# Optimization experiments

Measured on AMD Instinct MI355X. Metric: run time of the kernel, lower is better.

The kernel has to match this reference:

```python
import jax, jax.numpy as jnp
import numpy as np

E = 8       # num_experts
TOP_K = 2
H = 512     # hidden_size
DFF = 2048  # expert FFN inner dim (4*H)
B, S = 4, 2048


def setup_inputs() -> dict:
    key = jax.random.key(0)
    k0, k1, k2, k3 = jax.random.split(key, 4)
    return {
        "hidden_states": jax.random.normal(k0, (B, S, H), jnp.float32),
        # router gate: kaiming-ish init scaled by 0.01 (near-uniform routing)
        "gate_w": jax.random.normal(k1, (E, H), jnp.float32) * 0.01,
        "w1": jax.random.normal(k2, (E, H, DFF), jnp.float32) * (1.0 / np.sqrt(H)),
        "b1": jnp.zeros((E, DFF), jnp.float32),
        "w2": jax.random.normal(k3, (E, DFF, H), jnp.float32) * (1.0 / np.sqrt(DFF)),
        "b2": jnp.zeros((E, H), jnp.float32),
    }


def reference(hidden_states, gate_w, w1, b1, w2, b2):
    # hidden_states: (B, S, H)
    b, s, h = hidden_states.shape
    flat = hidden_states.reshape(-1, h)                 # (T, H), T = B*S

    # --- TopKRouter (eval mode: no gaussian noise) ---
    logits = flat @ gate_w.T                            # (T, E)
    top_vals, top_idx = jax.lax.top_k(logits, TOP_K)    # (T, K)
    top_w = jax.nn.softmax(top_vals, axis=-1)           # softmax over selected k only

    # combine[t, e] = routing weight of expert e for token t (0 if not selected).
    # top_k indices are distinct per token, so summing over k matches the
    # original masked scatter-add output[mask] += weight * expert_out.
    combine = jnp.sum(
        jax.nn.one_hot(top_idx, E, dtype=flat.dtype) * top_w[..., None], axis=1
    )                                                   # (T, E)

    # --- experts: dense compute per expert, weighted combine ---
    out = jnp.zeros_like(flat)
    for e in range(E):  # fixed small loop over experts (not a data dim)
        hdn = jax.nn.gelu(flat @ w1[e] + b1[e])         # (T, DFF)
        out = out + combine[:, e:e + 1] * (hdn @ w2[e] + b2[e])
    return out.reshape(b, s, h)
```

## Files before the change

kernel.cpp:

```cpp
#include <hip/hip_runtime.h>
#include <hip/hip_bf16.h>

#define E_    8
#define H_    512
#define DFF_  2048
#define T_    8192
#define NSLOT (2 * T_)

typedef float  f32x4  __attribute__((ext_vector_type(4)));
typedef short  bf16x8 __attribute__((ext_vector_type(8)));

static __device__ __forceinline__ ushort f2bf(float f) {
  union { float f; unsigned u; } v; v.f = f;
  unsigned r = v.u + 0x7FFFu + ((v.u >> 16) & 1u);
  return (ushort)(r >> 16);
}

static __device__ __forceinline__ void gload16(const void* g, void* l) {
  __builtin_amdgcn_global_load_lds((const __attribute__((address_space(1))) void*)g,
                                   (__attribute__((address_space(3))) void*)l, 16, 0, 0);
}

static __device__ __forceinline__ void transpose_body(
    const float* __restrict__ in, ushort* __restrict__ out, int R, int C,
    int bx, int by, int e, float tile[64][65], int t) {
  int r0 = by * 64, c0 = bx * 64;
  int row = t >> 2, seg = t & 3;
  const float* src = in + ((size_t)e * R + r0 + row) * C + c0 + seg * 16;
#pragma unroll
  for (int i = 0; i < 4; ++i) {
    float4 v = *(const float4*)(src + i * 4);
    tile[row][seg * 16 + i * 4 + 0] = v.x;
    tile[row][seg * 16 + i * 4 + 1] = v.y;
    tile[row][seg * 16 + i * 4 + 2] = v.z;
    tile[row][seg * 16 + i * 4 + 3] = v.w;
  }
  __syncthreads();
  int c = t >> 2;
  ushort vals[16];
#pragma unroll
  for (int j = 0; j < 16; ++j) vals[j] = f2bf(tile[seg * 16 + j][c]);
  ushort* dst = out + ((size_t)e * C + c0 + c) * R + r0 + seg * 16;
  *(uint4*)(dst)     = *(uint4*)&vals[0];
  *(uint4*)(dst + 8) = *(uint4*)&vals[8];
}

__global__ void prep_kernel(const float* __restrict__ x, const float* __restrict__ gw,
                            const float* __restrict__ w1, const float* __restrict__ w2,
                            ushort* __restrict__ xb, float* __restrict__ slotw,
                            int* __restrict__ slote, ushort* __restrict__ w1t,
                            ushort* __restrict__ w2t, float* __restrict__ out) {
  __shared__ float tile[64][65];
  int bid = blockIdx.x;
  int tid = threadIdx.x;
  if (bid < 2048) {
    int tokn = bid * 4 + (tid >> 6);
    int lane = tid & 63;
    const float4* xr = (const float4*)(x + (size_t)tokn * H_ + lane * 8);
    float4 x0 = xr[0], x1 = xr[1];
    ushort v[8] = {f2bf(x0.x), f2bf(x0.y), f2bf(x0.z), f2bf(x0.w),
                   f2bf(x1.x), f2bf(x1.y), f2bf(x1.z), f2bf(x1.w)};
    *(uint4*)(xb + (size_t)tokn * H_ + lane * 8) = *(uint4*)v;
    float acc[E_];
#pragma unroll
    for (int e = 0; e < E_; ++e) {
      const float4* gr = (const float4*)(gw + e * H_ + lane * 8);
      float4 g0 = gr[0], g1 = gr[1];
      acc[e] = x0.x*g0.x + x0.y*g0.y + x0.z*g0.z + x0.w*g0.w
             + x1.x*g1.x + x1.y*g1.y + x1.z*g1.z + x1.w*g1.w;
    }
#pragma unroll
    for (int e = 0; e < E_; ++e) {
#pragma unroll
      for (int off = 32; off; off >>= 1)
        acc[e] += __shfl_xor(acc[e], off);
    }
    if (lane == 0) {
      float v1 = -1e30f, v2 = -1e30f; int i1 = 0, i2 = 0;
#pragma unroll
      for (int e = 0; e < E_; ++e) {
        float vv = acc[e];
        if (vv > v1)      { v2 = v1; i2 = i1; v1 = vv; i1 = e; }
        else if (vv > v2) { v2 = vv; i2 = e; }
      }
      float ex = expf(v2 - v1);
      float inv = 1.0f / (1.0f + ex);
      slote[2 * tokn] = i1;     slotw[2 * tokn] = inv;
      slote[2 * tokn + 1] = i2; slotw[2 * tokn + 1] = ex * inv;
    }
  } else if (bid < 4096) {
    float* p = out + (size_t)(bid - 2048) * 2048 + tid * 8;
    float4 z = {0.f, 0.f, 0.f, 0.f};
    *(float4*)(p) = z;
    *(float4*)(p + 4) = z;
  } else if (bid < 6144) {
    int blk = bid - 4096;
    int bx = blk & 31, by = (blk >> 5) & 7, e = blk >> 8;
    transpose_body(w1, w1t, H_, DFF_, bx, by, e, tile, tid);
  } else {
    int blk = bid - 6144;
    int bx = blk & 7, by = (blk >> 3) & 31, e = blk >> 8;
    transpose_body(w2, w2t, DFF_, H_, bx, by, e, tile, tid);
  }
}

__global__ __launch_bounds__(1024) void listbuild_kernel(
    const int* __restrict__ slote, int* __restrict__ counts, int* __restrict__ lslot) {
  int tid = threadIdx.x, lane = tid & 63, wv = tid >> 6;
  int base = tid * 16;
  int myexp[16];
  unsigned char cnt[E_] = {0, 0, 0, 0, 0, 0, 0, 0};
#pragma unroll
  for (int i = 0; i < 16; ++i) {
    int e = slote[base + i];
    myexp[i] = e;
    cnt[e]++;
  }
  unsigned long long lo = 0, hi = 0;
#pragma unroll
  for (int e = 0; e < 4; ++e) {
    lo |= (unsigned long long)cnt[e] << (16 * e);
    hi |= (unsigned long long)cnt[e + 4] << (16 * e);
  }
  unsigned long long mylo = lo, myhi = hi;
#pragma unroll
  for (int off = 1; off < 64; off <<= 1) {
    unsigned long long tl = __shfl_up(lo, off);
    unsigned long long th = __shfl_up(hi, off);
    if (lane >= off) { lo += tl; hi += th; }
  }
  __shared__ unsigned long long wtotlo[16], wtothi[16];
  __shared__ unsigned long long wbaselo[16], wbasehi[16];
  if (lane == 63) { wtotlo[wv] = lo; wtothi[wv] = hi; }
  __syncthreads();
  if (tid == 0) {
    unsigned long long rl = 0, rh = 0;
#pragma unroll
    for (int w2 = 0; w2 < 16; ++w2) {
      wbaselo[w2] = rl; wbasehi[w2] = rh;
      rl += wtotlo[w2]; rh += wtothi[w2];
    }
#pragma unroll
    for (int e = 0; e < 4; ++e) {
      counts[e]     = (int)((rl >> (16 * e)) & 0xFFFF);
      counts[e + 4] = (int)((rh >> (16 * e)) & 0xFFFF);
    }
  }
  __syncthreads();
  unsigned long long exlo = wbaselo[wv] + lo - mylo;
  unsigned long long exhi = wbasehi[wv] + hi - myhi;
  int pos[E_];
#pragma unroll
  for (int e = 0; e < 4; ++e) {
    pos[e]     = (int)((exlo >> (16 * e)) & 0xFFFF);
    pos[e + 4] = (int)((exhi >> (16 * e)) & 0xFFFF);
  }
#pragma unroll
  for (int i = 0; i < 16; ++i) {
    int e = myexp[i];
    lslot[e * T_ + pos[e]] = base + i;
    pos[e]++;
  }
}

__global__ __launch_bounds__(256, 2) void gemm1_kernel(
    const ushort* __restrict__ xb, const ushort* __restrict__ w1t,
    const float* __restrict__ b1, const int* __restrict__ counts,
    const int* __restrict__ lslot, ushort* __restrict__ hdn, int c0, int DC) {
  int bid = blockIdx.x;
  int e = bid & (E_ - 1);
  int nx = DC / 128;
  int bx = (bid >> 3) % nx;
  int by = (bid >> 3) / nx;
  int cnt = counts[e];
  int m0 = by * 128;
  if (m0 >= cnt) return;
  int n0 = c0 + bx * 128;

  __shared__ ushort sA[128 * 64];
  __shared__ ushort sB[128 * 64];
  int tid = threadIdx.x, lane = tid & 63, wid = tid >> 6;
  int wm = wid >> 1, wn = wid & 1;
  const int* lst = lslot + e * T_;
  const ushort* w1e = w1t + (size_t)e * DFF_ * H_;

  int lrow = lane >> 3;
  int scol = ((lane & 7) ^ lrow) * 8;

  const ushort* asrc[4]; const ushort* bsrc[4];
#pragma unroll
  for (int is = 0; is < 4; ++is) {
    int row = (wid * 4 + is) * 8 + lrow;
    int r = m0 + row; if (r > cnt - 1) r = cnt - 1;
    asrc[is] = xb + (size_t)(lst[r] >> 1) * H_ + scol;
    bsrc[is] = w1e + (size_t)(n0 + row) * H_ + scol;
  }

  f32x4 acc[4][4];
#pragma unroll
  for (int i = 0; i < 4; ++i)
#pragma unroll
    for (int j = 0; j < 4; ++j) acc[i][j] = (f32x4){0.f, 0.f, 0.f, 0.f};

  for (int k0 = 0; k0 < H_; k0 += 64) {
    __syncthreads();
#pragma unroll
    for (int is = 0; is < 4; ++is) {
      gload16(asrc[is] + k0, &sA[(wid * 4 + is) * 512]);
      gload16(bsrc[is] + k0, &sB[(wid * 4 + is) * 512]);
    }
    __syncthreads();
#pragma unroll
    for (int s = 0; s < 2; ++s) {
      bf16x8 af[4], bfr[4];
#pragma unroll
      for (int i = 0; i < 4; ++i) {
        int row = wm * 64 + i * 16 + (lane & 15);
        af[i] = *(const bf16x8*)(&sA[row * 64 + (((s * 4 + (lane >> 4)) ^ (row & 7)) * 8)]);
      }
#pragma unroll
      for (int i = 0; i < 4; ++i) {
        int row = wn * 64 + i * 16 + (lane & 15);
        bfr[i] = *(const bf16x8*)(&sB[row * 64 + (((s * 4 + (lane >> 4)) ^ (row & 7)) * 8)]);
      }
#pragma unroll
      for (int i = 0; i < 4; ++i)
#pragma unroll
        for (int j = 0; j < 4; ++j)
          acc[i][j] = __builtin_amdgcn_mfma_f32_16x16x32_bf16(af[i], bfr[j], acc[i][j], 0, 0, 0);
    }
  }

  int cl = lane & 15, rg = lane >> 4;
  float b1v[4];
#pragma unroll
  for (int j = 0; j < 4; ++j) b1v[j] = b1[e * DFF_ + n0 + wn * 64 + j * 16 + cl];
#pragma unroll
  for (int i = 0; i < 4; ++i) {
    int rbase = m0 + wm * 64 + i * 16 + rg * 4;
#pragma unroll
    for (int r = 0; r < 4; ++r) {
      int gr = rbase + r;
      if (gr < cnt) {
        ushort* hrow = hdn + (size_t)lst[gr] * DC + (n0 - c0) + wn * 64 + cl;
#pragma unroll
        for (int j = 0; j < 4; ++j) {
          float v = acc[i][j][r] + b1v[j];
          float t2 = v + 0.044715f * v * v * v;
          float exv = __expf(1.5957691216057308f * t2);
          float th = 1.0f - 2.0f / (exv + 1.0f);
          hrow[j * 16] = f2bf(0.5f * v * (1.0f + th));
        }
      }
    }
  }
}

__global__ __launch_bounds__(256, 2) void gemm2_kernel(
    const ushort* __restrict__ hdn, const ushort* __restrict__ w2t,
    const float* __restrict__ b2, const float* __restrict__ slotw,
    const int* __restrict__ counts, const int* __restrict__ lslot,
    float* __restrict__ out, int c0, int DC, int addb) {
  int bid = blockIdx.x;
  int e = bid & (E_ - 1);
  const int nx = H_ / 128;
  int bx = (bid >> 3) % nx;
  int by = (bid >> 3) / nx;
  int cnt = counts[e];
  int m0 = by * 64;
  if (m0 >= cnt) return;
  int n0 = bx * 128;

  __shared__ ushort sA[64 * 64];
  __shared__ ushort sB[128 * 64];
  int tid = threadIdx.x, lane = tid & 63, wid = tid >> 6;
  int wm = wid >> 1, wn = wid & 1;
  const int* lst = lslot + e * T_;
  const ushort* w2e = w2t + (size_t)e * H_ * DFF_ + c0;

  int lrow = lane >> 3;
  int scol = ((lane & 7) ^ lrow) * 8;

  const ushort* asrc[2]; const ushort* bsrc[4];
#pragma unroll
  for (int is = 0; is < 2; ++is) {
    int row = (wid * 2 + is) * 8 + lrow;
    int r = m0 + row; if (r > cnt - 1) r = cnt - 1;
    asrc[is] = hdn + (size_t)lst[r] * DC + scol;
  }
#pragma unroll
  for (int is = 0; is < 4; ++is) {
    int row = (wid * 4 + is) * 8 + lrow;
    bsrc[is] = w2e + (size_t)(n0 + row) * DFF_ + scol;
  }

  f32x4 acc[2][4];
#pragma unroll
  for (int i = 0; i < 2; ++i)
#pragma unroll
    for (int j = 0; j < 4; ++j) acc[i][j] = (f32x4){0.f, 0.f, 0.f, 0.f};

  for (int k0 = 0; k0 < DC; k0 += 64) {
    __syncthreads();
#pragma unroll
    for (int is = 0; is < 2; ++is)
      gload16(asrc[is] + k0, &sA[(wid * 2 + is) * 512]);
#pragma unroll
    for (int is = 0; is < 4; ++is)
      gload16(bsrc[is] + k0, &sB[(wid * 4 + is) * 512]);
    __syncthreads();
#pragma unroll
    for (int s = 0; s < 2; ++s) {
      bf16x8 af[2], bfr[4];
#pragma unroll
      for (int i = 0; i < 2; ++i) {
        int row = wm * 32 + i * 16 + (lane & 15);
        af[i] = *(const bf16x8*)(&sA[row * 64 + (((s * 4 + (lane >> 4)) ^ (row & 7)) * 8)]);
      }
#pragma unroll
      for (int j = 0; j < 4; ++j) {
        int row = wn * 64 + j * 16 + (lane & 15);
        bfr[j] = *(const bf16x8*)(&sB[row * 64 + (((s * 4 + (lane >> 4)) ^ (row & 7)) * 8)]);
      }
#pragma unroll
      for (int i = 0; i < 2; ++i)
#pragma unroll
        for (int j = 0; j < 4; ++j)
          acc[i][j] = __builtin_amdgcn_mfma_f32_16x16x32_bf16(af[i], bfr[j], acc[i][j], 0, 0, 0);
    }
  }

  int cl = lane & 15, rg = lane >> 4;
  float b2v[4];
#pragma unroll
  for (int j = 0; j < 4; ++j)
    b2v[j] = addb ? b2[e * H_ + n0 + wn * 64 + j * 16 + cl] : 0.0f;
#pragma unroll
  for (int i = 0; i < 2; ++i) {
    int rbase = m0 + wm * 32 + i * 16 + rg * 4;
#pragma unroll
    for (int r = 0; r < 4; ++r) {
      int gr = rbase + r;
      if (gr < cnt) {
        int slot = lst[gr];
        float wgt = slotw[slot];
        float* orow = out + (size_t)(slot >> 1) * H_ + n0 + wn * 64 + cl;
#pragma unroll
        for (int j = 0; j < 4; ++j)
          atomicAdd(&orow[j * 16], wgt * (acc[i][j][r] + b2v[j]));
      }
    }
  }
}

extern "C" void kernel_launch(void* const* d_in, const int* in_sizes, int n_in,
                              void* d_out, int out_size, void* d_ws, size_t ws_size,
                              hipStream_t stream) {
  const float* x  = (const float*)d_in[0];
  const float* gw = (const float*)d_in[1];
  const float* w1 = (const float*)d_in[2];
  const float* b1 = (const float*)d_in[3];
  const float* w2 = (const float*)d_in[4];
  const float* b2 = (const float*)d_in[5];
  float* out = (float*)d_out;

  char* ws = (char*)d_ws;
  size_t off = 0;
  auto alloc = [&](size_t bytes) -> void* {
    void* p = ws + off; off += (bytes + 255) & ~(size_t)255; return p;
  };
  int*    counts = (int*)alloc(256);
  int*    lslot  = (int*)alloc((size_t)E_ * T_ * 4);
  float*  slotw  = (float*)alloc((size_t)NSLOT * 4);
  int*    slote  = (int*)alloc((size_t)NSLOT * 4);
  ushort* w1t    = (ushort*)alloc((size_t)E_ * DFF_ * H_ * 2);
  ushort* w2t    = (ushort*)alloc((size_t)E_ * H_ * DFF_ * 2);
  ushort* xb     = (ushort*)alloc((size_t)T_ * H_ * 2);

  int NC = 1;
  while (NC < 16 && off + (size_t)NSLOT * (DFF_ / NC) * 2 > ws_size) NC *= 2;
  int DC = DFF_ / NC;
  ushort* hdn = (ushort*)alloc((size_t)NSLOT * DC * 2);

  prep_kernel<<<8192, 256, 0, stream>>>(x, gw, w1, w2, xb, slotw, slote, w1t, w2t, out);
  listbuild_kernel<<<1, 1024, 0, stream>>>(slote, counts, lslot);

  for (int c = 0; c < NC; ++c) {
    gemm1_kernel<<<E_ * (DC / 128) * (T_ / 128), 256, 0, stream>>>(
        xb, w1t, b1, counts, lslot, hdn, c * DC, DC);
    gemm2_kernel<<<E_ * (H_ / 128) * (T_ / 64), 256, 0, stream>>>(
        hdn, w2t, b2, slotw, counts, lslot, out, c * DC, DC, c == NC - 1);
  }
}
```

Measured before the change: 162.0 us.

## Store hidden activations expert-contiguous and enlarge gemm2 M-tile to 256 rows

The expert hidden buffer is now indexed by a per-expert base offset plus the list position instead of by slot id, so each expert's rows are contiguous. gemm1 writes to and gemm2 reads from these sequential rows rather than gathering through the slot list. gemm2's tile grows from 64x128 to 256x128 with 4 waves each covering 64 rows across all 128 columns, and its launch bound drops to one block per SIMD. This raises reuse of the w2 tile per block, at the cost of more registers, lower occupancy and fewer blocks in the grid.

```diff
diff --git a/kernel.cpp b/kernel.cpp
--- a/kernel.cpp
+++ b/kernel.cpp
@@ -105,7 +105,8 @@
 }
 
 __global__ __launch_bounds__(1024) void listbuild_kernel(
-    const int* __restrict__ slote, int* __restrict__ counts, int* __restrict__ lslot) {
+    const int* __restrict__ slote, int* __restrict__ counts, int* __restrict__ ebase,
+    int* __restrict__ lslot) {
   int tid = threadIdx.x, lane = tid & 63, wv = tid >> 6;
   int base = tid * 16;
   int myexp[16];
@@ -140,10 +141,16 @@
       wbaselo[w2] = rl; wbasehi[w2] = rh;
       rl += wtotlo[w2]; rh += wtothi[w2];
     }
+    int run = 0;
 #pragma unroll
     for (int e = 0; e < 4; ++e) {
-      counts[e]     = (int)((rl >> (16 * e)) & 0xFFFF);
-      counts[e + 4] = (int)((rh >> (16 * e)) & 0xFFFF);
+      int tot = (int)((rl >> (16 * e)) & 0xFFFF);
+      counts[e] = tot; ebase[e] = run; run += tot;
+    }
+#pragma unroll
+    for (int e = 0; e < 4; ++e) {
+      int tot = (int)((rh >> (16 * e)) & 0xFFFF);
+      counts[e + 4] = tot; ebase[e + 4] = run; run += tot;
     }
   }
   __syncthreads();
@@ -166,7 +173,8 @@
 __global__ __launch_bounds__(256, 2) void gemm1_kernel(
     const ushort* __restrict__ xb, const ushort* __restrict__ w1t,
     const float* __restrict__ b1, const int* __restrict__ counts,
-    const int* __restrict__ lslot, ushort* __restrict__ hdn, int c0, int DC) {
+    const int* __restrict__ ebase, const int* __restrict__ lslot,
+    ushort* __restrict__ hdn, int c0, int DC) {
   int bid = blockIdx.x;
   int e = bid & (E_ - 1);
   int nx = DC / 128;
@@ -176,6 +184,7 @@
   int m0 = by * 128;
   if (m0 >= cnt) return;
   int n0 = c0 + bx * 128;
+  int eb = ebase[e];
 
   __shared__ ushort sA[128 * 64];
   __shared__ ushort sB[128 * 64];
@@ -242,7 +251,7 @@
     for (int r = 0; r < 4; ++r) {
       int gr = rbase + r;
       if (gr < cnt) {
-        ushort* hrow = hdn + (size_t)lst[gr] * DC + (n0 - c0) + wn * 64 + cl;
+        ushort* hrow = hdn + (size_t)(eb + gr) * DC + (n0 - c0) + wn * 64 + cl;
 #pragma unroll
         for (int j = 0; j < 4; ++j) {
           float v = acc[i][j][r] + b1v[j];
@@ -256,37 +265,38 @@
   }
 }
 
-__global__ __launch_bounds__(256, 2) void gemm2_kernel(
+__global__ __launch_bounds__(256, 1) void gemm2_kernel(
     const ushort* __restrict__ hdn, const ushort* __restrict__ w2t,
     const float* __restrict__ b2, const float* __restrict__ slotw,
-    const int* __restrict__ counts, const int* __restrict__ lslot,
-    float* __restrict__ out, int c0, int DC, int addb) {
+    const int* __restrict__ counts, const int* __restrict__ ebase,
+    const int* __restrict__ lslot, float* __restrict__ out,
+    int c0, int DC, int addb) {
   int bid = blockIdx.x;
   int e = bid & (E_ - 1);
   const int nx = H_ / 128;
   int bx = (bid >> 3) % nx;
   int by = (bid >> 3) / nx;
   int cnt = counts[e];
-  int m0 = by * 64;
+  int m0 = by * 256;
   if (m0 >= cnt) return;
   int n0 = bx * 128;
-
-  __shared__ ushort sA[64 * 64];
+  int eb = ebase[e];
+
+  __shared__ ushort sA[256 * 64];
   __shared__ ushort sB[128 * 64];
   int tid = threadIdx.x, lane = tid & 63, wid = tid >> 6;
-  int wm = wid >> 1, wn = wid & 1;
   const int* lst = lslot + e * T_;
   const ushort* w2e = w2t + (size_t)e * H_ * DFF_ + c0;
 
   int lrow = lane >> 3;
   int scol = ((lane & 7) ^ lrow) * 8;
 
-  const ushort* asrc[2]; const ushort* bsrc[4];
-#pragma unroll
-  for (int is = 0; is < 2; ++is) {
-    int row = (wid * 2 + is) * 8 + lrow;
+  const ushort* asrc[8]; const ushort* bsrc[4];
+#pragma unroll
+  for (int is = 0; is < 8; ++is) {
+    int row = (wid * 8 + is) * 8 + lrow;
     int r = m0 + row; if (r > cnt - 1) r = cnt - 1;
-    asrc[is] = hdn + (size_t)lst[r] * DC + scol;
+    asrc[is] = hdn + (size_t)(eb + r) * DC + scol;
   }
 #pragma unroll
   for (int is = 0; is < 4; ++is) {
@@ -294,59 +304,59 @@
     bsrc[is] = w2e + (size_t)(n0 + row) * DFF_ + scol;
   }
 
-  f32x4 acc[2][4];
-#pragma unroll
-  for (int i = 0; i < 2; ++i)
-#pragma unroll
-    for (int j = 0; j < 4; ++j) acc[i][j] = (f32x4){0.f, 0.f, 0.f, 0.f};
+  f32x4 acc[4][8];
+#pragma unroll
+  for (int i = 0; i < 4; ++i)
+#pragma unroll
+    for (int j = 0; j < 8; ++j) acc[i][j] = (f32x4){0.f, 0.f, 0.f, 0.f};
 
   for (int k0 = 0; k0 < DC; k0 += 64) {
     __syncthreads();
 #pragma unroll
-    for (int is = 0; is < 2; ++is)
-      gload16(asrc[is] + k0, &sA[(wid * 2 + is) * 512]);
+    for (int is = 0; is < 8; ++is)
+      gload16(asrc[is] + k0, &sA[(wid * 8 + is) * 512]);
 #pragma unroll
     for (int is = 0; is < 4; ++is)
       gload16(bsrc[is] + k0, &sB[(wid * 4 + is) * 512]);
     __syncthreads();
 #pragma unroll
     for (int s = 0; s < 2; ++s) {
-      bf16x8 af[2], bfr[4];
-#pragma unroll
-      for (int i = 0; i < 2; ++i) {
-        int row = wm * 32 + i * 16 + (lane & 15);
+      bf16x8 af[4], bfr[8];
+#pragma unroll
+      for (int i = 0; i < 4; ++i) {
+        int row = wid * 64 + i * 16 + (lane & 15);
         af[i] = *(const bf16x8*)(&sA[row * 64 + (((s * 4 + (lane >> 4)) ^ (row & 7)) * 8)]);
       }
 #pragma unroll
-      for (int j = 0; j < 4; ++j) {
-        int row = wn * 64 + j * 16 + (lane & 15);
+      for (int j = 0; j < 8; ++j) {
+        int row = j * 16 + (lane & 15);
         bfr[j] = *(const bf16x8*)(&sB[row * 64 + (((s * 4 + (lane >> 4)) ^ (row & 7)) * 8)]);
       }
 #pragma unroll
-      for (int i = 0; i < 2; ++i)
-#pragma unroll
-        for (int j = 0; j < 4; ++j)
+      for (int i = 0; i < 4; ++i)
+#pragma unroll
+        for (int j = 0; j < 8; ++j)
           acc[i][j] = __builtin_amdgcn_mfma_f32_16x16x32_bf16(af[i], bfr[j], acc[i][j], 0, 0, 0);
     }
   }
 
   int cl = lane & 15, rg = lane >> 4;
-  float b2v[4];
-#pragma unroll
-  for (int j = 0; j < 4; ++j)
-    b2v[j] = addb ? b2[e * H_ + n0 + wn * 64 + j * 16 + cl] : 0.0f;
-#pragma unroll
-  for (int i = 0; i < 2; ++i) {
-    int rbase = m0 + wm * 32 + i * 16 + rg * 4;
+  float b2v[8];
+#pragma unroll
+  for (int j = 0; j < 8; ++j)
+    b2v[j] = addb ? b2[e * H_ + n0 + j * 16 + cl] : 0.0f;
+#pragma unroll
+  for (int i = 0; i < 4; ++i) {
+    int rbase = m0 + wid * 64 + i * 16 + rg * 4;
 #pragma unroll
     for (int r = 0; r < 4; ++r) {
       int gr = rbase + r;
       if (gr < cnt) {
         int slot = lst[gr];
         float wgt = slotw[slot];
-        float* orow = out + (size_t)(slot >> 1) * H_ + n0 + wn * 64 + cl;
-#pragma unroll
-        for (int j = 0; j < 4; ++j)
+        float* orow = out + (size_t)(slot >> 1) * H_ + n0 + cl;
+#pragma unroll
+        for (int j = 0; j < 8; ++j)
           atomicAdd(&orow[j * 16], wgt * (acc[i][j][r] + b2v[j]));
       }
     }
@@ -370,6 +380,7 @@
     void* p = ws + off; off += (bytes + 255) & ~(size_t)255; return p;
   };
   int*    counts = (int*)alloc(256);
+  int*    ebase  = (int*)alloc(256);
   int*    lslot  = (int*)alloc((size_t)E_ * T_ * 4);
   float*  slotw  = (float*)alloc((size_t)NSLOT * 4);
   int*    slote  = (int*)alloc((size_t)NSLOT * 4);
@@ -383,12 +394,12 @@
   ushort* hdn = (ushort*)alloc((size_t)NSLOT * DC * 2);
 
   prep_kernel<<<8192, 256, 0, stream>>>(x, gw, w1, w2, xb, slotw, slote, w1t, w2t, out);
-  listbuild_kernel<<<1, 1024, 0, stream>>>(slote, counts, lslot);
+  listbuild_kernel<<<1, 1024, 0, stream>>>(slote, counts, ebase, lslot);
 
   for (int c = 0; c < NC; ++c) {
     gemm1_kernel<<<E_ * (DC / 128) * (T_ / 128), 256, 0, stream>>>(
-        xb, w1t, b1, counts, lslot, hdn, c * DC, DC);
-    gemm2_kernel<<<E_ * (H_ / 128) * (T_ / 64), 256, 0, stream>>>(
-        hdn, w2t, b2, slotw, counts, lslot, out, c * DC, DC, c == NC - 1);
-  }
-}
+        xb, w1t, b1, counts, ebase, lslot, hdn, c * DC, DC);
+    gemm2_kernel<<<E_ * (H_ / 128) * (T_ / 256), 256, 0, stream>>>(
+        hdn, w2t, b2, slotw, counts, ebase, lslot, out, c * DC, DC, c == NC - 1);
+  }
+}
```

After: 225.5 us. 39.2% more time.

## Store hidden activations expert-contiguous and shrink gemm1 M tile to 64

Applied to the files above, without the earlier changes.

Adds per-expert base offsets from the list build and writes gemm1's GELU outputs into an expert-contiguous hidden buffer, so gemm2 reads A rows sequentially instead of gathering through the slot list. gemm1's row tile drops from 128 to 64, matching gemm2 and doubling the grid. The smaller tile reduces wasted rows at each expert's tail but halves weight reuse per block and raises weight reload traffic.

```diff
diff --git a/kernel.cpp b/kernel.cpp
--- a/kernel.cpp
+++ b/kernel.cpp
@@ -105,7 +105,8 @@
 }
 
 __global__ __launch_bounds__(1024) void listbuild_kernel(
-    const int* __restrict__ slote, int* __restrict__ counts, int* __restrict__ lslot) {
+    const int* __restrict__ slote, int* __restrict__ counts, int* __restrict__ ebase,
+    int* __restrict__ lslot) {
   int tid = threadIdx.x, lane = tid & 63, wv = tid >> 6;
   int base = tid * 16;
   int myexp[16];
@@ -140,10 +141,16 @@
       wbaselo[w2] = rl; wbasehi[w2] = rh;
       rl += wtotlo[w2]; rh += wtothi[w2];
     }
+    int run = 0;
 #pragma unroll
     for (int e = 0; e < 4; ++e) {
-      counts[e]     = (int)((rl >> (16 * e)) & 0xFFFF);
-      counts[e + 4] = (int)((rh >> (16 * e)) & 0xFFFF);
+      int tot = (int)((rl >> (16 * e)) & 0xFFFF);
+      counts[e] = tot; ebase[e] = run; run += tot;
+    }
+#pragma unroll
+    for (int e = 0; e < 4; ++e) {
+      int tot = (int)((rh >> (16 * e)) & 0xFFFF);
+      counts[e + 4] = tot; ebase[e + 4] = run; run += tot;
     }
   }
   __syncthreads();
@@ -166,18 +173,20 @@
 __global__ __launch_bounds__(256, 2) void gemm1_kernel(
     const ushort* __restrict__ xb, const ushort* __restrict__ w1t,
     const float* __restrict__ b1, const int* __restrict__ counts,
-    const int* __restrict__ lslot, ushort* __restrict__ hdn, int c0, int DC) {
+    const int* __restrict__ ebase, const int* __restrict__ lslot,
+    ushort* __restrict__ hdn, int c0, int DC) {
   int bid = blockIdx.x;
   int e = bid & (E_ - 1);
   int nx = DC / 128;
   int bx = (bid >> 3) % nx;
   int by = (bid >> 3) / nx;
   int cnt = counts[e];
-  int m0 = by * 128;
+  int m0 = by * 64;
   if (m0 >= cnt) return;
   int n0 = c0 + bx * 128;
-
-  __shared__ ushort sA[128 * 64];
+  int eb = ebase[e];
+
+  __shared__ ushort sA[64 * 64];
   __shared__ ushort sB[128 * 64];
   int tid = threadIdx.x, lane = tid & 63, wid = tid >> 6;
   int wm = wid >> 1, wn = wid & 1;
@@ -187,44 +196,49 @@
   int lrow = lane >> 3;
   int scol = ((lane & 7) ^ lrow) * 8;
 
-  const ushort* asrc[4]; const ushort* bsrc[4];
+  const ushort* asrc[2]; const ushort* bsrc[4];
+#pragma unroll
+  for (int is = 0; is < 2; ++is) {
+    int row = (wid * 2 + is) * 8 + lrow;
+    int r = m0 + row; if (r > cnt - 1) r = cnt - 1;
+    asrc[is] = xb + (size_t)(lst[r] >> 1) * H_ + scol;
+  }
 #pragma unroll
   for (int is = 0; is < 4; ++is) {
     int row = (wid * 4 + is) * 8 + lrow;
-    int r = m0 + row; if (r > cnt - 1) r = cnt - 1;
-    asrc[is] = xb + (size_t)(lst[r] >> 1) * H_ + scol;
     bsrc[is] = w1e + (size_t)(n0 + row) * H_ + scol;
   }
 
-  f32x4 acc[4][4];
-#pragma unroll
-  for (int i = 0; i < 4; ++i)
+  f32x4 acc[2][4];
+#pragma unroll
+  for (int i = 0; i < 2; ++i)
 #pragma unroll
     for (int j = 0; j < 4; ++j) acc[i][j] = (f32x4){0.f, 0.f, 0.f, 0.f};
 
   for (int k0 = 0; k0 < H_; k0 += 64) {
     __syncthreads();
 #pragma unroll
-    for (int is = 0; is < 4; ++is) {
-      gload16(asrc[is] + k0, &sA[(wid * 4 + is) * 512]);
+    for (int is = 0; is < 2; ++is)
+      gload16(asrc[is] + k0, &sA[(wid * 2 + is) * 512]);
+#pragma unroll
+    for (int is = 0; is < 4; ++is)
       gload16(bsrc[is] + k0, &sB[(wid * 4 + is) * 512]);
-    }
     __syncthreads();
 #pragma unroll
     for (int s = 0; s < 2; ++s) {
-      bf16x8 af[4], bfr[4];
-#pragma unroll
-      for (int i = 0; i < 4; ++i) {
-        int row = wm * 64 + i * 16 + (lane & 15);
+      bf16x8 af[2], bfr[4];
+#pragma unroll
+      for (int i = 0; i < 2; ++i) {
+        int row = wm * 32 + i * 16 + (lane & 15);
         af[i] = *(const bf16x8*)(&sA[row * 64 + (((s * 4 + (lane >> 4)) ^ (row & 7)) * 8)]);
       }
 #pragma unroll
-      for (int i = 0; i < 4; ++i) {
-        int row = wn * 64 + i * 16 + (lane & 15);
-        bfr[i] = *(const bf16x8*)(&sB[row * 64 + (((s * 4 + (lane >> 4)) ^ (row & 7)) * 8)]);
-      }
-#pragma unroll
-      for (int i = 0; i < 4; ++i)
+      for (int j = 0; j < 4; ++j) {
+        int row = wn * 64 + j * 16 + (lane & 15);
+        bfr[j] = *(const bf16x8*)(&sB[row * 64 + (((s * 4 + (lane >> 4)) ^ (row & 7)) * 8)]);
+      }
+#pragma unroll
+      for (int i = 0; i < 2; ++i)
 #pragma unroll
         for (int j = 0; j < 4; ++j)
           acc[i][j] = __builtin_amdgcn_mfma_f32_16x16x32_bf16(af[i], bfr[j], acc[i][j], 0, 0, 0);
@@ -236,13 +250,13 @@
 #pragma unroll
   for (int j = 0; j < 4; ++j) b1v[j] = b1[e * DFF_ + n0 + wn * 64 + j * 16 + cl];
 #pragma unroll
-  for (int i = 0; i < 4; ++i) {
-    int rbase = m0 + wm * 64 + i * 16 + rg * 4;
+  for (int i = 0; i < 2; ++i) {
+    int rbase = m0 + wm * 32 + i * 16 + rg * 4;
 #pragma unroll
     for (int r = 0; r < 4; ++r) {
       int gr = rbase + r;
       if (gr < cnt) {
-        ushort* hrow = hdn + (size_t)lst[gr] * DC + (n0 - c0) + wn * 64 + cl;
+        ushort* hrow = hdn + (size_t)(eb + gr) * DC + (n0 - c0) + wn * 64 + cl;
 #pragma unroll
         for (int j = 0; j < 4; ++j) {
           float v = acc[i][j][r] + b1v[j];
@@ -259,8 +273,9 @@
 __global__ __launch_bounds__(256, 2) void gemm2_kernel(
     const ushort* __restrict__ hdn, const ushort* __restrict__ w2t,
     const float* __restrict__ b2, const float* __restrict__ slotw,
-    const int* __restrict__ counts, const int* __restrict__ lslot,
-    float* __restrict__ out, int c0, int DC, int addb) {
+    const int* __restrict__ counts, const int* __restrict__ ebase,
+    const int* __restrict__ lslot, float* __restrict__ out,
+    int c0, int DC, int addb) {
   int bid = blockIdx.x;
   int e = bid & (E_ - 1);
   const int nx = H_ / 128;
@@ -270,6 +285,7 @@
   int m0 = by * 64;
   if (m0 >= cnt) return;
   int n0 = bx * 128;
+  int eb = ebase[e];
 
   __shared__ ushort sA[64 * 64];
   __shared__ ushort sB[128 * 64];
@@ -286,7 +302,7 @@
   for (int is = 0; is < 2; ++is) {
     int row = (wid * 2 + is) * 8 + lrow;
     int r = m0 + row; if (r > cnt - 1) r = cnt - 1;
-    asrc[is] = hdn + (size_t)lst[r] * DC + scol;
+    asrc[is] = hdn + (size_t)(eb + r) * DC + scol;
   }
 #pragma unroll
   for (int is = 0; is < 4; ++is) {
@@ -370,6 +386,7 @@
     void* p = ws + off; off += (bytes + 255) & ~(size_t)255; return p;
   };
   int*    counts = (int*)alloc(256);
+  int*    ebase  = (int*)alloc(256);
   int*    lslot  = (int*)alloc((size_t)E_ * T_ * 4);
   float*  slotw  = (float*)alloc((size_t)NSLOT * 4);
   int*    slote  = (int*)alloc((size_t)NSLOT * 4);
@@ -383,12 +400,12 @@
   ushort* hdn = (ushort*)alloc((size_t)NSLOT * DC * 2);
 
   prep_kernel<<<8192, 256, 0, stream>>>(x, gw, w1, w2, xb, slotw, slote, w1t, w2t, out);
-  listbuild_kernel<<<1, 1024, 0, stream>>>(slote, counts, lslot);
+  listbuild_kernel<<<1, 1024, 0, stream>>>(slote, counts, ebase, lslot);
 
   for (int c = 0; c < NC; ++c) {
-    gemm1_kernel<<<E_ * (DC / 128) * (T_ / 128), 256, 0, stream>>>(
-        xb, w1t, b1, counts, lslot, hdn, c * DC, DC);
+    gemm1_kernel<<<E_ * (DC / 128) * (T_ / 64), 256, 0, stream>>>(
+        xb, w1t, b1, counts, ebase, lslot, hdn, c * DC, DC);
     gemm2_kernel<<<E_ * (H_ / 128) * (T_ / 64), 256, 0, stream>>>(
-        hdn, w2t, b2, slotw, counts, lslot, out, c * DC, DC, c == NC - 1);
-  }
-}
+        hdn, w2t, b2, slotw, counts, ebase, lslot, out, c * DC, DC, c == NC - 1);
+  }
+}
```

After: 158.5 us. 2.1% less time.
